# Performance work log

Hardware: AMD Instinct MI355X
Metric: run time of the kernel (lower is better)

The kernel has to match this reference:

```python
import jax, jax.numpy as jnp
import numpy as np

B, N, F, K = 64, 4096, 128, 64
N_STEP = 4
EPS_VAR = 1e-5


def setup_inputs() -> dict:
    key = jax.random.key(0)
    k1, k2, k3 = jax.random.split(key, 3)
    emb_in = jax.random.normal(k1, (B, N, F), dtype=jnp.float32)
    # number of valid nodes per sample; must be > K so init indices are valid
    batch_nb_nodes = jax.random.randint(k2, (B,), K + 1, N + 1).astype(jnp.int32)
    mask = (jnp.arange(N)[None, :] < batch_nb_nodes[:, None]).astype(jnp.float32)
    fc_w = jax.random.normal(k3, (1, F), dtype=jnp.float32) / np.float32(np.sqrt(F))
    fc_b = jnp.zeros((1,), dtype=jnp.float32)
    init_idx = jnp.arange(K, dtype=jnp.int32)  # replaces np.random.choice
    return {"emb_in": emb_in, "mask": mask, "fc_w": fc_w, "fc_b": fc_b,
            "batch_nb_nodes": batch_nb_nodes, "init_idx": init_idx}


def spatialnorm(emb, batch_nb_nodes, mask):
    # masked per-sample, per-feature standardization over the node axis
    n = batch_nb_nodes.astype(emb.dtype)[:, None, None]        # [B,1,1]
    m = mask[:, :, None]                                       # [B,N,1]
    mean = (emb * m).sum(axis=1, keepdims=True) / n            # [B,1,F]
    var = (((emb - mean) ** 2) * m).sum(axis=1, keepdims=True) / n
    x = (emb - mean) / jnp.sqrt(var + EPS_VAR) * m
    return x, mean, var


def expectation(x, mu):
    # squared L2 dists via expansion; avoids the [B,N,K,F] diff tensor
    x2 = (x * x).sum(-1)                                       # [B,N]
    m2 = (mu * mu).sum(-1)                                     # [B,K]
    xm = jnp.einsum('bnf,bkf->bnk', x, mu)                     # [B,N,K]
    norm = x2[:, :, None] - 2.0 * xm + m2[:, None, :]
    likelihood = jnp.exp(-0.5 * norm) + 1e-20
    P = likelihood / (likelihood.sum(axis=2, keepdims=True) + 1e-40)
    return P


def maximization(x, P):
    # mu = P^T X  (note: original does NOT divide by cluster mass)
    return jnp.einsum('bnk,bnf->bkf', P, x)


def reference(emb_in, mask, fc_w, fc_b, batch_nb_nodes, init_idx):
    x, _, _ = spatialnorm(emb_in, batch_nb_nodes, mask)
    mu = x[:, init_idx]                                        # [B,K,F]
    for _ in range(N_STEP):
        P = expectation(x, mu)
        mu = maximization(x, P)
    out = jnp.einsum('bkf,of->bko', mu, fc_w) + fc_b           # fc(mu): [B,K,1]
    out = out[..., 0].mean(axis=1)                             # [B]
    return jax.nn.sigmoid(out)
```

## Files before the change

### kernel.cpp

```cpp
#include <hip/hip_runtime.h>
#include <math.h>

#define BB 64
#define NN 4096
#define FF 128
#define KK 64
#define TILE 128
#define NT 4
#define NSTEP 4

__device__ __forceinline__ float dot4acc(float4 a, float4 b, float s) {
    return fmaf(a.w, b.w, fmaf(a.z, b.z, fmaf(a.y, b.y, fmaf(a.x, b.x, s))));
}

__global__ void k_stats_part(const float* __restrict__ emb, const int* __restrict__ nbv,
                             float* __restrict__ spart) {
    int b = blockIdx.y, s = blockIdx.x;
    int nb = nbv[b];
    int t = threadIdx.x;
    int c = t & 31, rr = t >> 5;
    int n0 = s * 512;
    int n1 = min(n0 + 512, nb);
    float4 s1 = {0,0,0,0}, s2 = {0,0,0,0};
    const float4* base = (const float4*)(emb + (size_t)b * NN * FF);
    for (int n = n0 + rr; n < n1; n += 8) {
        float4 e = base[(size_t)n * 32 + c];
        s1.x += e.x; s1.y += e.y; s1.z += e.z; s1.w += e.w;
        s2.x += e.x*e.x; s2.y += e.y*e.y; s2.z += e.z*e.z; s2.w += e.w*e.w;
    }
    __shared__ __align__(16) float4 r1[8][32];
    __shared__ __align__(16) float4 r2[8][32];
    r1[rr][c] = s1; r2[rr][c] = s2;
    __syncthreads();
    if (t < 32) {
        float4 a1 = r1[0][t], a2 = r2[0][t];
        #pragma unroll
        for (int r = 1; r < 8; ++r) {
            float4 u = r1[r][t], v = r2[r][t];
            a1.x+=u.x; a1.y+=u.y; a1.z+=u.z; a1.w+=u.w;
            a2.x+=v.x; a2.y+=v.y; a2.z+=v.z; a2.w+=v.w;
        }
        ((float4*)(spart + ((size_t)(b*8+s)*2 + 0)*FF))[t] = a1;
        ((float4*)(spart + ((size_t)(b*8+s)*2 + 1)*FF))[t] = a2;
    }
}

__global__ void k_stats_fin(const float* __restrict__ spart, const int* __restrict__ nbv,
                            float* __restrict__ meanp, float* __restrict__ rstdp) {
    int b = blockIdx.x, f = threadIdx.x;
    float s1 = 0.f, s2 = 0.f;
    #pragma unroll
    for (int s = 0; s < 8; ++s) {
        s1 += spart[((size_t)(b*8+s)*2 + 0)*FF + f];
        s2 += spart[((size_t)(b*8+s)*2 + 1)*FF + f];
    }
    float nb = (float)nbv[b];
    float mean = s1 / nb;
    float var = s2 / nb - mean * mean;
    meanp[b*FF + f] = mean;
    rstdp[b*FF + f] = rsqrtf(var + 1e-5f);
}

__global__ void k_init(const float* __restrict__ emb, const int* __restrict__ nbv,
                       const int* __restrict__ init_idx,
                       const float* __restrict__ meanp, const float* __restrict__ rstdp,
                       float* __restrict__ mu) {
    size_t i = (size_t)blockIdx.x * 256 + threadIdx.x;
    int f = (int)(i & 127);
    int k = (int)((i >> 7) & 63);
    int b = (int)(i >> 13);
    int row = init_idx[k];
    float v = 0.f;
    if (row < nbv[b]) {
        float e = emb[((size_t)b * NN + row) * FF + f];
        v = (e - meanp[b*FF + f]) * rstdp[b*FF + f];
    }
    mu[i] = v;
}

__global__ __launch_bounds__(512) void k_em(const float* __restrict__ emb,
                                            const int* __restrict__ nbv,
                                            const float* __restrict__ meanp,
                                            const float* __restrict__ rstdp,
                                            const float* __restrict__ mu_in,
                                            float* __restrict__ partial) {
    __shared__ __align__(16) float4 xs[TILE][32];
    __shared__ __align__(16) float4 mus[KK][32];
    __shared__ __align__(16) float sp[TILE][64];
    __shared__ __align__(16) float mean_s[FF];
    __shared__ __align__(16) float rstd_s[FF];
    __shared__ float x2s[TILE];
    __shared__ float m2s[KK];

    int b = blockIdx.y, t0 = blockIdx.x;
    int nb = nbv[b];
    int t = threadIdx.x;
    int lane = t & 63, w = t >> 6;

    if (t < FF) mean_s[t] = meanp[b*FF + t];
    else if (t < 2*FF) rstd_s[t - FF] = rstdp[b*FF + (t - FF)];

    {
        const float4* src = (const float4*)(mu_in + (size_t)b * KK * FF);
        #pragma unroll
        for (int j = 0; j < 4; ++j) {
            int g = t + 512 * j;
            int row = g >> 5, c = g & 31;
            float4 v = src[g];
            mus[row][c ^ ((row >> 2) & 7)] = v;
            float q = v.x*v.x + v.y*v.y + v.z*v.z + v.w*v.w;
            q += __shfl_xor(q, 16); q += __shfl_xor(q, 8);
            q += __shfl_xor(q, 4);  q += __shfl_xor(q, 2); q += __shfl_xor(q, 1);
            if ((t & 31) == 0) m2s[row] = q;
        }
    }

    float4 acc0 = {0,0,0,0}, acc1 = {0,0,0,0}, acc2 = {0,0,0,0}, acc3 = {0,0,0,0};
    __syncthreads();

    int nTiles = (nb + TILE - 1) / TILE;
    for (int tt = t0; tt < nTiles; tt += NT) {
        int row0 = tt * TILE;
        {
            const float4* erow = (const float4*)(emb + ((size_t)b * NN + row0) * FF);
            #pragma unroll
            for (int j = 0; j < 8; ++j) {
                int g = t + 512 * j;
                int r = g >> 5, c = g & 31;
                int n = row0 + r;
                float4 v = {0,0,0,0};
                if (n < nb) {
                    float4 e = erow[g];
                    float4 mn = ((float4*)mean_s)[c];
                    float4 rs = ((float4*)rstd_s)[c];
                    v.x = (e.x - mn.x) * rs.x;
                    v.y = (e.y - mn.y) * rs.y;
                    v.z = (e.z - mn.z) * rs.z;
                    v.w = (e.w - mn.w) * rs.w;
                }
                xs[r][c ^ ((r >> 2) & 7)] = v;
                float q = v.x*v.x + v.y*v.y + v.z*v.z + v.w*v.w;
                q += __shfl_xor(q, 16); q += __shfl_xor(q, 8);
                q += __shfl_xor(q, 4);  q += __shfl_xor(q, 2); q += __shfl_xor(q, 1);
                if ((t & 31) == 0) x2s[r] = q;
            }
        }
        __syncthreads();

        {
            int lr = lane & 15;
            int kq = w & 3, rh = w >> 2;
            int rbase = rh * 64 + lr * 4;
            int k4 = kq * 4 + (lane >> 4);
            int aswz = lr & 7;
            int bswz = k4 & 7;
            float4 s0 = {0,0,0,0}, s1 = {0,0,0,0}, s2 = {0,0,0,0}, s3 = {0,0,0,0};
            #pragma unroll 2
            for (int fc = 0; fc < 32; ++fc) {
                int as = fc ^ aswz, bs = fc ^ bswz;
                float4 a0 = xs[rbase + 0][as];
                float4 a1 = xs[rbase + 1][as];
                float4 a2 = xs[rbase + 2][as];
                float4 a3 = xs[rbase + 3][as];
                float4 b0 = mus[k4*4 + 0][bs];
                float4 b1 = mus[k4*4 + 1][bs];
                float4 b2 = mus[k4*4 + 2][bs];
                float4 b3 = mus[k4*4 + 3][bs];
                s0.x = dot4acc(a0, b0, s0.x); s0.y = dot4acc(a0, b1, s0.y);
                s0.z = dot4acc(a0, b2, s0.z); s0.w = dot4acc(a0, b3, s0.w);
                s1.x = dot4acc(a1, b0, s1.x); s1.y = dot4acc(a1, b1, s1.y);
                s1.z = dot4acc(a1, b2, s1.z); s1.w = dot4acc(a1, b3, s1.w);
                s2.x = dot4acc(a2, b0, s2.x); s2.y = dot4acc(a2, b1, s2.y);
                s2.z = dot4acc(a2, b2, s2.z); s2.w = dot4acc(a2, b3, s2.w);
                s3.x = dot4acc(a3, b0, s3.x); s3.y = dot4acc(a3, b1, s3.y);
                s3.z = dot4acc(a3, b2, s3.z); s3.w = dot4acc(a3, b3, s3.w);
            }
            ((float4*)&sp[rbase + 0][0])[k4 ^ aswz] = s0;
            ((float4*)&sp[rbase + 1][0])[k4 ^ aswz] = s1;
            ((float4*)&sp[rbase + 2][0])[k4 ^ aswz] = s2;
            ((float4*)&sp[rbase + 3][0])[k4 ^ aswz] = s3;
        }
        __syncthreads();

        for (int i = 0; i < 16; ++i) {
            int r = w * 16 + i;
            int swz = (r >> 2) & 7;
            int col = (((lane >> 2) ^ swz) << 2) | (lane & 3);
            float s = sp[r][col];
            float norm = x2s[r] - 2.f * s + m2s[lane];
            float lik = expf(-0.5f * norm) + 1e-20f;
            float tot = lik;
            tot += __shfl_xor(tot, 1);  tot += __shfl_xor(tot, 2);
            tot += __shfl_xor(tot, 4);  tot += __shfl_xor(tot, 8);
            tot += __shfl_xor(tot, 16); tot += __shfl_xor(tot, 32);
            sp[r][col] = lik / (tot + 1e-40f);
        }
        __syncthreads();

        {
            int kg = lane & 15, fg = lane >> 4;
            int fslot = w * 4 + fg;
            #pragma unroll 4
            for (int n = 0; n < TILE; ++n) {
                int swz = (n >> 2) & 7;
                float4 p4 = *(const float4*)&sp[n][(kg ^ swz) << 2];
                float4 x4 = xs[n][fslot ^ swz];
                acc0.x = fmaf(p4.x, x4.x, acc0.x); acc0.y = fmaf(p4.x, x4.y, acc0.y);
                acc0.z = fmaf(p4.x, x4.z, acc0.z); acc0.w = fmaf(p4.x, x4.w, acc0.w);
                acc1.x = fmaf(p4.y, x4.x, acc1.x); acc1.y = fmaf(p4.y, x4.y, acc1.y);
                acc1.z = fmaf(p4.y, x4.z, acc1.z); acc1.w = fmaf(p4.y, x4.w, acc1.w);
                acc2.x = fmaf(p4.z, x4.x, acc2.x); acc2.y = fmaf(p4.z, x4.y, acc2.y);
                acc2.z = fmaf(p4.z, x4.z, acc2.z); acc2.w = fmaf(p4.z, x4.w, acc2.w);
                acc3.x = fmaf(p4.w, x4.x, acc3.x); acc3.y = fmaf(p4.w, x4.y, acc3.y);
                acc3.z = fmaf(p4.w, x4.z, acc3.z); acc3.w = fmaf(p4.w, x4.w, acc3.w);
            }
        }
        __syncthreads();
    }

    {
        int kg = lane & 15, fg = lane >> 4;
        float* pp = partial + (((size_t)t0 * BB + b) * KK) * FF;
        int f = w * 16 + fg * 4;
        *((float4*)(pp + (size_t)(kg*4 + 0) * FF + f)) = acc0;
        *((float4*)(pp + (size_t)(kg*4 + 1) * FF + f)) = acc1;
        *((float4*)(pp + (size_t)(kg*4 + 2) * FF + f)) = acc2;
        *((float4*)(pp + (size_t)(kg*4 + 3) * FF + f)) = acc3;
    }
}

__global__ void k_reduce(const float* __restrict__ partial, float* __restrict__ mu_out) {
    size_t i = (size_t)blockIdx.x * 256 + threadIdx.x;
    float s = 0.f;
    #pragma unroll
    for (int tpart = 0; tpart < NT; ++tpart)
        s += partial[(size_t)tpart * BB * KK * FF + i];
    mu_out[i] = s;
}

__global__ void k_final(const float* __restrict__ mu, const float* __restrict__ fc_w,
                        const float* __restrict__ fc_b, float* __restrict__ out) {
    int b = blockIdx.x, t = threadIdx.x;
    int k = t >> 2, q = t & 3;
    const float* m = mu + ((size_t)b * KK + k) * FF + q * 32;
    const float* wv = fc_w + q * 32;
    float s = 0.f;
    #pragma unroll
    for (int i = 0; i < 32; ++i) s = fmaf(m[i], wv[i], s);
    s += __shfl_xor(s, 1); s += __shfl_xor(s, 2);
    __shared__ float kd[KK];
    if (q == 0) kd[k] = s;
    __syncthreads();
    if (t < 64) {
        float v = kd[t];
        v += __shfl_xor(v, 1);  v += __shfl_xor(v, 2);  v += __shfl_xor(v, 4);
        v += __shfl_xor(v, 8);  v += __shfl_xor(v, 16); v += __shfl_xor(v, 32);
        if (t == 0) {
            float o = v / (float)KK + fc_b[0];
            out[b] = 1.f / (1.f + expf(-o));
        }
    }
}

extern "C" void kernel_launch(void* const* d_in, const int* in_sizes, int n_in,
                              void* d_out, int out_size, void* d_ws, size_t ws_size,
                              hipStream_t stream) {
    const float* emb      = (const float*)d_in[0];
    const float* fc_w     = (const float*)d_in[2];
    const float* fc_b     = (const float*)d_in[3];
    const int*   nbv      = (const int*)d_in[4];
    const int*   init_idx = (const int*)d_in[5];
    float* out = (float*)d_out;

    float* wsf   = (float*)d_ws;
    float* meanp = wsf;
    float* rstdp = meanp + BB*FF;
    float* spart = rstdp + BB*FF;
    float* muA   = spart + (size_t)BB*8*2*FF;
    float* muB   = muA + (size_t)BB*KK*FF;
    float* part  = muB + (size_t)BB*KK*FF;

    k_stats_part<<<dim3(8, BB), 256, 0, stream>>>(emb, nbv, spart);
    k_stats_fin<<<BB, 128, 0, stream>>>(spart, nbv, meanp, rstdp);
    k_init<<<(BB*KK*FF)/256, 256, 0, stream>>>(emb, nbv, init_idx, meanp, rstdp, muA);

    for (int step = 0; step < NSTEP; ++step) {
        const float* mu_in = (step & 1) ? muB : muA;
        float* mu_out      = (step & 1) ? muA : muB;
        k_em<<<dim3(NT, BB), 512, 0, stream>>>(emb, nbv, meanp, rstdp, mu_in, part);
        k_reduce<<<(BB*KK*FF)/256, 256, 0, stream>>>(part, mu_out);
    }
    k_final<<<BB, 256, 0, stream>>>(muA, fc_w, fc_b, out);
}
```

Before: 885.3 us.

## Give each EM block a single tile and reduce mu via atomics

The EM kernel now launches one 1024-thread block per 128-node tile, (N/TILE)×B blocks instead of 4×B persistent blocks. Partial mu results are accumulated straight into the output with float atomic adds, after a zeroing kernel, which removes the partial buffer and the separate reduce kernel. The stats pass is also split into 32 chunks per sample to raise parallelism. The aim is to fill the GPU with far more blocks. The cost is a large number of atomics, order-dependent floating-point summation, and reloading mu into shared memory for every tile.

```diff
diff --git a/kernel.cpp b/kernel.cpp
--- a/kernel.cpp
+++ b/kernel.cpp
@@ -6,8 +6,8 @@
 #define FF 128
 #define KK 64
 #define TILE 128
-#define NT 4
 #define NSTEP 4
+#define SPB 32
 
 __device__ __forceinline__ float dot4acc(float4 a, float4 b, float s) {
     return fmaf(a.w, b.w, fmaf(a.z, b.z, fmaf(a.y, b.y, fmaf(a.x, b.x, s))));
@@ -19,8 +19,8 @@
     int nb = nbv[b];
     int t = threadIdx.x;
     int c = t & 31, rr = t >> 5;
-    int n0 = s * 512;
-    int n1 = min(n0 + 512, nb);
+    int n0 = s * (NN / SPB);
+    int n1 = min(n0 + NN / SPB, nb);
     float4 s1 = {0,0,0,0}, s2 = {0,0,0,0};
     const float4* base = (const float4*)(emb + (size_t)b * NN * FF);
     for (int n = n0 + rr; n < n1; n += 8) {
@@ -40,8 +40,8 @@
             a1.x+=u.x; a1.y+=u.y; a1.z+=u.z; a1.w+=u.w;
             a2.x+=v.x; a2.y+=v.y; a2.z+=v.z; a2.w+=v.w;
         }
-        ((float4*)(spart + ((size_t)(b*8+s)*2 + 0)*FF))[t] = a1;
-        ((float4*)(spart + ((size_t)(b*8+s)*2 + 1)*FF))[t] = a2;
+        ((float4*)(spart + ((size_t)(b*SPB+s)*2 + 0)*FF))[t] = a1;
+        ((float4*)(spart + ((size_t)(b*SPB+s)*2 + 1)*FF))[t] = a2;
     }
 }
 
@@ -49,10 +49,9 @@
                             float* __restrict__ meanp, float* __restrict__ rstdp) {
     int b = blockIdx.x, f = threadIdx.x;
     float s1 = 0.f, s2 = 0.f;
-    #pragma unroll
-    for (int s = 0; s < 8; ++s) {
-        s1 += spart[((size_t)(b*8+s)*2 + 0)*FF + f];
-        s2 += spart[((size_t)(b*8+s)*2 + 1)*FF + f];
+    for (int s = 0; s < SPB; ++s) {
+        s1 += spart[((size_t)(b*SPB+s)*2 + 0)*FF + f];
+        s2 += spart[((size_t)(b*SPB+s)*2 + 1)*FF + f];
     }
     float nb = (float)nbv[b];
     float mean = s1 / nb;
@@ -78,164 +77,138 @@
     mu[i] = v;
 }
 
-__global__ __launch_bounds__(512) void k_em(const float* __restrict__ emb,
-                                            const int* __restrict__ nbv,
-                                            const float* __restrict__ meanp,
-                                            const float* __restrict__ rstdp,
-                                            const float* __restrict__ mu_in,
-                                            float* __restrict__ partial) {
+__global__ void k_zero(float* __restrict__ p) {
+    size_t i = (size_t)blockIdx.x * 1024 + threadIdx.x;
+    ((float4*)p)[i] = make_float4(0.f, 0.f, 0.f, 0.f);
+}
+
+__global__ __launch_bounds__(1024, 4) void k_em2(const float* __restrict__ emb,
+                                                 const int* __restrict__ nbv,
+                                                 const float* __restrict__ meanp,
+                                                 const float* __restrict__ rstdp,
+                                                 const float* __restrict__ mu_in,
+                                                 float* __restrict__ mu_out) {
     __shared__ __align__(16) float4 xs[TILE][32];
     __shared__ __align__(16) float4 mus[KK][32];
     __shared__ __align__(16) float sp[TILE][64];
-    __shared__ __align__(16) float mean_s[FF];
-    __shared__ __align__(16) float rstd_s[FF];
     __shared__ float x2s[TILE];
     __shared__ float m2s[KK];
 
-    int b = blockIdx.y, t0 = blockIdx.x;
+    int b = blockIdx.y, tt = blockIdx.x;
     int nb = nbv[b];
+    int row0 = tt * TILE;
+    if (row0 >= nb) return;
     int t = threadIdx.x;
     int lane = t & 63, w = t >> 6;
 
-    if (t < FF) mean_s[t] = meanp[b*FF + t];
-    else if (t < 2*FF) rstd_s[t - FF] = rstdp[b*FF + (t - FF)];
-
     {
         const float4* src = (const float4*)(mu_in + (size_t)b * KK * FF);
         #pragma unroll
-        for (int j = 0; j < 4; ++j) {
-            int g = t + 512 * j;
-            int row = g >> 5, c = g & 31;
+        for (int j = 0; j < 2; ++j) {
+            int g = t + 1024 * j;
+            int r = g >> 5, c = g & 31;
             float4 v = src[g];
-            mus[row][c ^ ((row >> 2) & 7)] = v;
+            mus[r][c ^ ((r >> 2) & 7)] = v;
             float q = v.x*v.x + v.y*v.y + v.z*v.z + v.w*v.w;
             q += __shfl_xor(q, 16); q += __shfl_xor(q, 8);
             q += __shfl_xor(q, 4);  q += __shfl_xor(q, 2); q += __shfl_xor(q, 1);
-            if ((t & 31) == 0) m2s[row] = q;
-        }
-    }
-
-    float4 acc0 = {0,0,0,0}, acc1 = {0,0,0,0}, acc2 = {0,0,0,0}, acc3 = {0,0,0,0};
-    __syncthreads();
-
-    int nTiles = (nb + TILE - 1) / TILE;
-    for (int tt = t0; tt < nTiles; tt += NT) {
-        int row0 = tt * TILE;
-        {
-            const float4* erow = (const float4*)(emb + ((size_t)b * NN + row0) * FF);
-            #pragma unroll
-            for (int j = 0; j < 8; ++j) {
-                int g = t + 512 * j;
-                int r = g >> 5, c = g & 31;
-                int n = row0 + r;
-                float4 v = {0,0,0,0};
-                if (n < nb) {
-                    float4 e = erow[g];
-                    float4 mn = ((float4*)mean_s)[c];
-                    float4 rs = ((float4*)rstd_s)[c];
-                    v.x = (e.x - mn.x) * rs.x;
-                    v.y = (e.y - mn.y) * rs.y;
-                    v.z = (e.z - mn.z) * rs.z;
-                    v.w = (e.w - mn.w) * rs.w;
-                }
-                xs[r][c ^ ((r >> 2) & 7)] = v;
-                float q = v.x*v.x + v.y*v.y + v.z*v.z + v.w*v.w;
-                q += __shfl_xor(q, 16); q += __shfl_xor(q, 8);
-                q += __shfl_xor(q, 4);  q += __shfl_xor(q, 2); q += __shfl_xor(q, 1);
-                if ((t & 31) == 0) x2s[r] = q;
+            if ((t & 31) == 0) m2s[r] = q;
+        }
+    }
+
+    {
+        const float4* erow = (const float4*)(emb + ((size_t)b * NN + row0) * FF);
+        int c = t & 31;
+        float4 mn = ((const float4*)(meanp + b * FF))[c];
+        float4 rs = ((const float4*)(rstdp + b * FF))[c];
+        #pragma unroll
+        for (int j = 0; j < 4; ++j) {
+            int g = t + 1024 * j;
+            int r = g >> 5;
+            int n = row0 + r;
+            float4 v = {0,0,0,0};
+            if (n < nb) {
+                float4 e = erow[g];
+                v.x = (e.x - mn.x) * rs.x;
+                v.y = (e.y - mn.y) * rs.y;
+                v.z = (e.z - mn.z) * rs.z;
+                v.w = (e.w - mn.w) * rs.w;
             }
-        }
-        __syncthreads();
-
-        {
-            int lr = lane & 15;
-            int kq = w & 3, rh = w >> 2;
-            int rbase = rh * 64 + lr * 4;
-            int k4 = kq * 4 + (lane >> 4);
-            int aswz = lr & 7;
-            int bswz = k4 & 7;
-            float4 s0 = {0,0,0,0}, s1 = {0,0,0,0}, s2 = {0,0,0,0}, s3 = {0,0,0,0};
-            #pragma unroll 2
-            for (int fc = 0; fc < 32; ++fc) {
-                int as = fc ^ aswz, bs = fc ^ bswz;
-                float4 a0 = xs[rbase + 0][as];
-                float4 a1 = xs[rbase + 1][as];
-                float4 a2 = xs[rbase + 2][as];
-                float4 a3 = xs[rbase + 3][as];
-                float4 b0 = mus[k4*4 + 0][bs];
-                float4 b1 = mus[k4*4 + 1][bs];
-                float4 b2 = mus[k4*4 + 2][bs];
-                float4 b3 = mus[k4*4 + 3][bs];
-                s0.x = dot4acc(a0, b0, s0.x); s0.y = dot4acc(a0, b1, s0.y);
-                s0.z = dot4acc(a0, b2, s0.z); s0.w = dot4acc(a0, b3, s0.w);
-                s1.x = dot4acc(a1, b0, s1.x); s1.y = dot4acc(a1, b1, s1.y);
-                s1.z = dot4acc(a1, b2, s1.z); s1.w = dot4acc(a1, b3, s1.w);
-                s2.x = dot4acc(a2, b0, s2.x); s2.y = dot4acc(a2, b1, s2.y);
-                s2.z = dot4acc(a2, b2, s2.z); s2.w = dot4acc(a2, b3, s2.w);
-                s3.x = dot4acc(a3, b0, s3.x); s3.y = dot4acc(a3, b1, s3.y);
-                s3.z = dot4acc(a3, b2, s3.z); s3.w = dot4acc(a3, b3, s3.w);
-            }
-            ((float4*)&sp[rbase + 0][0])[k4 ^ aswz] = s0;
-            ((float4*)&sp[rbase + 1][0])[k4 ^ aswz] = s1;
-            ((float4*)&sp[rbase + 2][0])[k4 ^ aswz] = s2;
-            ((float4*)&sp[rbase + 3][0])[k4 ^ aswz] = s3;
-        }
-        __syncthreads();
-
-        for (int i = 0; i < 16; ++i) {
-            int r = w * 16 + i;
-            int swz = (r >> 2) & 7;
-            int col = (((lane >> 2) ^ swz) << 2) | (lane & 3);
-            float s = sp[r][col];
-            float norm = x2s[r] - 2.f * s + m2s[lane];
-            float lik = expf(-0.5f * norm) + 1e-20f;
-            float tot = lik;
-            tot += __shfl_xor(tot, 1);  tot += __shfl_xor(tot, 2);
-            tot += __shfl_xor(tot, 4);  tot += __shfl_xor(tot, 8);
-            tot += __shfl_xor(tot, 16); tot += __shfl_xor(tot, 32);
-            sp[r][col] = lik / (tot + 1e-40f);
-        }
-        __syncthreads();
-
-        {
-            int kg = lane & 15, fg = lane >> 4;
-            int fslot = w * 4 + fg;
-            #pragma unroll 4
-            for (int n = 0; n < TILE; ++n) {
-                int swz = (n >> 2) & 7;
-                float4 p4 = *(const float4*)&sp[n][(kg ^ swz) << 2];
-                float4 x4 = xs[n][fslot ^ swz];
-                acc0.x = fmaf(p4.x, x4.x, acc0.x); acc0.y = fmaf(p4.x, x4.y, acc0.y);
-                acc0.z = fmaf(p4.x, x4.z, acc0.z); acc0.w = fmaf(p4.x, x4.w, acc0.w);
-                acc1.x = fmaf(p4.y, x4.x, acc1.x); acc1.y = fmaf(p4.y, x4.y, acc1.y);
-                acc1.z = fmaf(p4.y, x4.z, acc1.z); acc1.w = fmaf(p4.y, x4.w, acc1.w);
-                acc2.x = fmaf(p4.z, x4.x, acc2.x); acc2.y = fmaf(p4.z, x4.y, acc2.y);
-                acc2.z = fmaf(p4.z, x4.z, acc2.z); acc2.w = fmaf(p4.z, x4.w, acc2.w);
-                acc3.x = fmaf(p4.w, x4.x, acc3.x); acc3.y = fmaf(p4.w, x4.y, acc3.y);
-                acc3.z = fmaf(p4.w, x4.z, acc3.z); acc3.w = fmaf(p4.w, x4.w, acc3.w);
-            }
-        }
-        __syncthreads();
-    }
-
-    {
-        int kg = lane & 15, fg = lane >> 4;
-        float* pp = partial + (((size_t)t0 * BB + b) * KK) * FF;
-        int f = w * 16 + fg * 4;
-        *((float4*)(pp + (size_t)(kg*4 + 0) * FF + f)) = acc0;
-        *((float4*)(pp + (size_t)(kg*4 + 1) * FF + f)) = acc1;
-        *((float4*)(pp + (size_t)(kg*4 + 2) * FF + f)) = acc2;
-        *((float4*)(pp + (size_t)(kg*4 + 3) * FF + f)) = acc3;
-    }
-}
-
-__global__ void k_reduce(const float* __restrict__ partial, float* __restrict__ mu_out) {
-    size_t i = (size_t)blockIdx.x * 256 + threadIdx.x;
-    float s = 0.f;
+            xs[r][c ^ ((r >> 2) & 7)] = v;
+            float q = v.x*v.x + v.y*v.y + v.z*v.z + v.w*v.w;
+            q += __shfl_xor(q, 16); q += __shfl_xor(q, 8);
+            q += __shfl_xor(q, 4);  q += __shfl_xor(q, 2); q += __shfl_xor(q, 1);
+            if ((t & 31) == 0) x2s[r] = q;
+        }
+    }
+    __syncthreads();
+
+    {
+        int wr = w & 7, wk = w >> 3;
+        int lr = lane & 7, lk = lane >> 3;
+        int r0 = wr * 16 + lr * 2;
+        int k4 = wk * 8 + lk;
+        int aswz = (r0 >> 2) & 7;
+        int bswz = k4 & 7;
+        float4 s0 = {0,0,0,0}, s1 = {0,0,0,0};
+        #pragma unroll 2
+        for (int fc = 0; fc < 32; ++fc) {
+            int as = fc ^ aswz, bs = fc ^ bswz;
+            float4 a0 = xs[r0 + 0][as];
+            float4 a1 = xs[r0 + 1][as];
+            float4 b0 = mus[k4*4 + 0][bs];
+            float4 b1 = mus[k4*4 + 1][bs];
+            float4 b2 = mus[k4*4 + 2][bs];
+            float4 b3 = mus[k4*4 + 3][bs];
+            s0.x = dot4acc(a0, b0, s0.x); s0.y = dot4acc(a0, b1, s0.y);
+            s0.z = dot4acc(a0, b2, s0.z); s0.w = dot4acc(a0, b3, s0.w);
+            s1.x = dot4acc(a1, b0, s1.x); s1.y = dot4acc(a1, b1, s1.y);
+            s1.z = dot4acc(a1, b2, s1.z); s1.w = dot4acc(a1, b3, s1.w);
+        }
+        ((float4*)&sp[r0 + 0][0])[k4 ^ aswz] = s0;
+        ((float4*)&sp[r0 + 1][0])[k4 ^ aswz] = s1;
+    }
+    __syncthreads();
+
     #pragma unroll
-    for (int tpart = 0; tpart < NT; ++tpart)
-        s += partial[(size_t)tpart * BB * KK * FF + i];
-    mu_out[i] = s;
+    for (int i = 0; i < 8; ++i) {
+        int r = w * 8 + i;
+        int swz = (r >> 2) & 7;
+        int col = (((lane >> 2) ^ swz) << 2) | (lane & 3);
+        float s = sp[r][col];
+        float norm = x2s[r] - 2.f * s + m2s[lane];
+        float lik = expf(-0.5f * norm) + 1e-20f;
+        float tot = lik;
+        tot += __shfl_xor(tot, 1);  tot += __shfl_xor(tot, 2);
+        tot += __shfl_xor(tot, 4);  tot += __shfl_xor(tot, 8);
+        tot += __shfl_xor(tot, 16); tot += __shfl_xor(tot, 32);
+        sp[r][col] = lik / (tot + 1e-40f);
+    }
+    __syncthreads();
+
+    {
+        int wf = w & 3, wk2 = w >> 2;
+        int lk = lane & 7, lf = lane >> 3;
+        int k0 = wk2 * 16 + lk * 2;
+        int fslot = wf * 8 + lf;
+        float4 a0 = {0,0,0,0}, a1 = {0,0,0,0};
+        #pragma unroll 4
+        for (int n = 0; n < TILE; ++n) {
+            int swz = (n >> 2) & 7;
+            float2 p = *(const float2*)&sp[n][((((k0 >> 2) ^ swz)) << 2) | (k0 & 3)];
+            float4 x4 = xs[n][fslot ^ swz];
+            a0.x = fmaf(p.x, x4.x, a0.x); a0.y = fmaf(p.x, x4.y, a0.y);
+            a0.z = fmaf(p.x, x4.z, a0.z); a0.w = fmaf(p.x, x4.w, a0.w);
+            a1.x = fmaf(p.y, x4.x, a1.x); a1.y = fmaf(p.y, x4.y, a1.y);
+            a1.z = fmaf(p.y, x4.z, a1.z); a1.w = fmaf(p.y, x4.w, a1.w);
+        }
+        float* d0 = mu_out + ((size_t)b * KK + k0) * FF + fslot * 4;
+        unsafeAtomicAdd(d0 + 0, a0.x); unsafeAtomicAdd(d0 + 1, a0.y);
+        unsafeAtomicAdd(d0 + 2, a0.z); unsafeAtomicAdd(d0 + 3, a0.w);
+        float* d1 = d0 + FF;
+        unsafeAtomicAdd(d1 + 0, a1.x); unsafeAtomicAdd(d1 + 1, a1.y);
+        unsafeAtomicAdd(d1 + 2, a1.z); unsafeAtomicAdd(d1 + 3, a1.w);
+    }
 }
 
 __global__ void k_final(const float* __restrict__ mu, const float* __restrict__ fc_w,
@@ -276,19 +249,19 @@
     float* meanp = wsf;
     float* rstdp = meanp + BB*FF;
     float* spart = rstdp + BB*FF;
-    float* muA   = spart + (size_t)BB*8*2*FF;
+    float* muA   = spart + (size_t)BB*SPB*2*FF;
     float* muB   = muA + (size_t)BB*KK*FF;
-    float* part  = muB + (size_t)BB*KK*FF;
-
-    k_stats_part<<<dim3(8, BB), 256, 0, stream>>>(emb, nbv, spart);
+
+    k_stats_part<<<dim3(SPB, BB), 256, 0, stream>>>(emb, nbv, spart);
     k_stats_fin<<<BB, 128, 0, stream>>>(spart, nbv, meanp, rstdp);
     k_init<<<(BB*KK*FF)/256, 256, 0, stream>>>(emb, nbv, init_idx, meanp, rstdp, muA);
 
+    const int zblocks = (BB*KK*FF/4) / 1024;
     for (int step = 0; step < NSTEP; ++step) {
         const float* mu_in = (step & 1) ? muB : muA;
         float* mu_out      = (step & 1) ? muA : muB;
-        k_em<<<dim3(NT, BB), 512, 0, stream>>>(emb, nbv, meanp, rstdp, mu_in, part);
-        k_reduce<<<(BB*KK*FF)/256, 256, 0, stream>>>(part, mu_out);
+        k_zero<<<zblocks, 1024, 0, stream>>>(mu_out);
+        k_em2<<<dim3(NN/TILE, BB), 1024, 0, stream>>>(emb, nbv, meanp, rstdp, mu_in, mu_out);
     }
     k_final<<<BB, 256, 0, stream>>>(muA, fc_w, fc_b, out);
 }
```

After: 1.097 ms. 23.9% more time.
